# Kernel tuning notes

Measured on AMD Instinct MI355X. Metric: run time of the kernel, lower is better.

## Reference

```python
import jax, jax.numpy as jnp
import numpy as np

ENT_SIZE = 100000; REL_SIZE = 500; ENT_DIM = 256; REL_DIM = 256; H = 256
E = 2048; S = 32; N = 1024; THRESHOLD = 1.0; EPS = 1e-5


def _xav(k, shape):
    fan_in = shape[-1]
    fan_out = shape[-2] if len(shape) > 1 else shape[-1]
    std = (2.0 / (fan_in + fan_out)) ** 0.5
    return jax.random.normal(k, shape, jnp.float32) * std


def setup_inputs() -> dict:
    key = jax.random.key(0)
    ks = jax.random.split(key, 16)
    inp = {}
    inp["neighbors"] = jax.random.randint(ks[0], (E, S), 0, ENT_SIZE)
    inp["pos_h"] = jax.random.randint(ks[1], (N,), 0, E)
    inp["pos_t"] = jax.random.randint(ks[2], (N,), 0, E)
    inp["pos_r"] = jax.random.randint(ks[3], (N,), 0, REL_SIZE)
    inp["neg_h"] = jax.random.randint(ks[4], (N,), 0, E)
    inp["neg_t"] = jax.random.randint(ks[5], (N,), 0, E)
    inp["neg_r"] = jax.random.randint(ks[6], (N,), 0, REL_SIZE)
    inp["ent_embed"] = _xav(ks[7], (ENT_SIZE + 1, ENT_DIM))
    inp["rel_embed"] = _xav(ks[8], (REL_SIZE, REL_DIM))
    inp["trans"] = _xav(ks[9], (2 * REL_SIZE, REL_DIM, ENT_DIM))
    inp["W_ih_f"] = _xav(ks[10], (4 * H, ENT_DIM)); inp["W_hh_f"] = _xav(ks[11], (4 * H, H))
    inp["W_ih_b"] = _xav(ks[12], (4 * H, ENT_DIM)); inp["W_hh_b"] = _xav(ks[13], (4 * H, H))
    inp["b_f"] = jnp.zeros((4 * H,), jnp.float32)
    inp["b_b"] = jnp.zeros((4 * H,), jnp.float32)
    inp["W_lin"] = _xav(ks[14], (ENT_DIM, 2 * H)); inp["b_lin"] = jnp.zeros((ENT_DIM,), jnp.float32)
    inp["gamma"] = jnp.ones((ENT_DIM,), jnp.float32); inp["beta"] = jnp.zeros((ENT_DIM,), jnp.float32)
    return inp


def _lstm_final(x, W_ih, W_hh, b):
    # x: [E,S,D] -> final hidden state [E,H] (PyTorch LSTM gate order i,f,g,o; b = b_ih+b_hh)
    h0 = jnp.zeros((x.shape[0], H), x.dtype)
    def step(carry, xt):
        h, c = carry
        g = xt @ W_ih.T + h @ W_hh.T + b  # [E,4H]
        i, f, gg, o = jnp.split(g, 4, axis=-1)
        c = jax.nn.sigmoid(f) * c + jax.nn.sigmoid(i) * jnp.tanh(gg)
        h = jax.nn.sigmoid(o) * jnp.tanh(c)
        return (h, c), None
    (h, _), _ = jax.lax.scan(step, (h0, h0), jnp.swapaxes(x, 0, 1))
    return h


def _context(ent_embed, neighbors, W_ih_f, W_hh_f, b_f, W_ih_b, W_hh_b, b_b, W_lin, b_lin, gamma, beta):
    x_seq = ent_embed[neighbors]  # [E,S,D]
    h_f = _lstm_final(x_seq, W_ih_f, W_hh_f, b_f)
    h_b = _lstm_final(x_seq[:, ::-1], W_ih_b, W_hh_b, b_b)
    lin = jnp.concatenate([h_f, h_b], -1) @ W_lin.T + b_lin  # [E,ENT_DIM]
    # BatchNorm1d in training mode: batch stats (biased variance)
    mu = lin.mean(0)
    var = lin.var(0)
    return jnp.tanh(gamma * (lin - mu) * jax.lax.rsqrt(var + EPS) + beta)


def _score(trans, rel_embed, ctx, h_idx, r_idx, t_idx):
    Wh = trans[r_idx]             # [N,REL_DIM,ENT_DIM] (grouped expert GEMV, batched)
    Wt = trans[r_idx + REL_SIZE]
    d = jnp.einsum('nre,ne->nr', Wh, ctx[h_idx]) - jnp.einsum('nre,ne->nr', Wt, ctx[t_idx])
    return jnp.linalg.norm(d + rel_embed[r_idx], axis=1)


def reference(neighbors, pos_h, pos_t, pos_r, neg_h, neg_t, neg_r,
              ent_embed, rel_embed, trans, W_ih_f, W_hh_f, W_ih_b, W_hh_b,
              b_f, b_b, W_lin, b_lin, gamma, beta):
    ctx = _context(ent_embed, neighbors, W_ih_f, W_hh_f, b_f, W_ih_b, W_hh_b, b_b,
                   W_lin, b_lin, gamma, beta)
    pos_n = _score(trans, rel_embed, ctx, pos_h, pos_r, pos_t)
    neg_n = _score(trans, rel_embed, ctx, neg_h, neg_r, neg_t)
    return jnp.sum(pos_n + jax.nn.relu(THRESHOLD - neg_n))
```

## Files before the change

### kernel.cpp

```cpp
#include <hip/hip_runtime.h>

constexpr int kE   = 2048;
constexpr int kS   = 32;
constexpr int kD   = 256;
constexpr int kK   = 512;
constexpr int kREL = 500;
constexpr int kN   = 1024;

typedef unsigned short u16;
typedef __attribute__((ext_vector_type(8))) _Float16 f16x8;
typedef __attribute__((ext_vector_type(4))) float    f32x4;
typedef __attribute__((ext_vector_type(4))) unsigned short us4;

static __device__ __forceinline__ u16 f2h(float f) {
  _Float16 h = (_Float16)f;
  return __builtin_bit_cast(u16, h);
}
static __device__ __forceinline__ float h2f(u16 v) {
  _Float16 h = __builtin_bit_cast(_Float16, v);
  return (float)h;
}
static __device__ __forceinline__ float sigf(float x) { return 1.f / (1.f + __expf(-x)); }
static __device__ __forceinline__ float tanhfast(float x) {
  float e = __expf(2.f * x);
  return 1.f - 2.f / (e + 1.f);
}

__global__ void prep_weights(const float* __restrict__ Wih_f, const float* __restrict__ Whh_f,
                             const float* __restrict__ Wih_b, const float* __restrict__ Whh_b,
                             const float* __restrict__ Wlin_in,
                             u16* __restrict__ Wihr, u16* __restrict__ Whhr,
                             u16* __restrict__ Wlin) {
  int idx = blockIdx.x * 256 + threadIdx.x;
  if (idx < 65536) {
    int d = idx >> 15;
    int j = (idx & 32767) >> 5;
    int k = (idx & 31) * 8;
    int g = (j >> 4) & 3, u = (j >> 6) * 16 + (j & 15);
    int R = g * 256 + u;
    const float* src = (d ? Wih_b : Wih_f) + R * 256 + k;
    ushort oa[8];
#pragma unroll
    for (int i = 0; i < 8; i++) oa[i] = f2h(src[i]);
    *(uint4*)((char*)Wihr + (size_t)idx * 16) = *(uint4*)oa;
  } else if (idx < 131072) {
    int i2 = idx - 65536;
    int d = i2 >> 15;
    int j = (i2 & 32767) >> 5;
    int k = (i2 & 31) * 8;
    int g = (j >> 4) & 3, u = (j >> 6) * 16 + (j & 15);
    int R = g * 256 + u;
    const float* src = (d ? Whh_b : Whh_f) + R * 256 + k;
    ushort oa[8];
#pragma unroll
    for (int i = 0; i < 8; i++) oa[i] = f2h(src[i]);
    *(uint4*)((char*)Whhr + (size_t)i2 * 16) = *(uint4*)oa;
  } else if (idx < 131072 + 16384) {
    int q = (idx - 131072) * 8;
#pragma unroll
    for (int i = 0; i < 8; i++) Wlin[q + i] = f2h(Wlin_in[q + i]);
  }
}

__global__ void gather_x(const int* __restrict__ neighbors, const float* __restrict__ ent,
                         u16* __restrict__ x16) {
  const int tot = kS * kE * kD / 4;
  for (int i = blockIdx.x * blockDim.x + threadIdx.x; i < tot; i += gridDim.x * blockDim.x) {
    int k4 = i & 63;
    int row = i >> 6;
    int e = row & (kE - 1);
    int s = row >> 11;
    int nb = neighbors[e * kS + s];
    float4 v = *(const float4*)(ent + (size_t)nb * kD + k4 * 4);
    ushort4 o;
    o.x = f2h(v.x); o.y = f2h(v.y); o.z = f2h(v.z); o.w = f2h(v.w);
    *(ushort4*)(x16 + (size_t)row * kD + k4 * 4) = o;
  }
}

__global__ __launch_bounds__(256) void xgemm(
    const u16* __restrict__ x16, const u16* __restrict__ Wihr,
    const float* __restrict__ b_f, const float* __restrict__ b_b,
    u16* __restrict__ gx, int t0, int T) {
  const int tid = threadIdx.x, lane = tid & 63, w = tid >> 6;
  const int l15 = lane & 15, lq = lane >> 4;
  const int row0 = blockIdx.x * 64;
  const int y = blockIdx.y;
  const int dir = blockIdx.z;
  const int tt = row0 >> 11;
  const int e0 = row0 & 2047;
  const int s = dir ? (31 - (t0 + tt)) : (t0 + tt);
  const u16* Ab = x16 + ((size_t)s * kE + e0) * kD;
  const int c0 = y * 256 + w * 64;
  const u16* Bb = Wihr + ((size_t)dir * 1024 + c0) * kD;
  const float* bd = dir ? b_b : b_f;
  const int u = (c0 >> 6) * 16 + l15;

  f32x4 acc[4][4];
#pragma unroll
  for (int n = 0; n < 4; n++) {
    float bv = bd[n * 256 + u];
#pragma unroll
    for (int m = 0; m < 4; m++) acc[m][n] = (f32x4){bv, bv, bv, bv};
  }

  const int klane = lq * 8;
#pragma unroll
  for (int ks = 0; ks < 8; ks++) {
    const int ka = ks * 32 + klane;
    f16x8 a[4], b[4];
#pragma unroll
    for (int m = 0; m < 4; m++)
      a[m] = *(const f16x8*)(Ab + (size_t)(m * 16 + l15) * kD + ka);
#pragma unroll
    for (int n = 0; n < 4; n++)
      b[n] = *(const f16x8*)(Bb + (size_t)(n * 16 + l15) * kD + ka);
#pragma unroll
    for (int m = 0; m < 4; m++)
#pragma unroll
      for (int n = 0; n < 4; n++)
        acc[m][n] = __builtin_amdgcn_mfma_f32_16x16x32_f16(a[m], b[n], acc[m][n], 0, 0, 0);
  }

  u16* out = gx + (((size_t)dir * T + tt) * kE) * 1024;
#pragma unroll
  for (int m = 0; m < 4; m++)
#pragma unroll
    for (int r = 0; r < 4; r++) {
      int e = e0 + m * 16 + lq * 4 + r;
      us4 o;
      o[0] = f2h(acc[m][0][r]); o[1] = f2h(acc[m][1][r]);
      o[2] = f2h(acc[m][2][r]); o[3] = f2h(acc[m][3][r]);
      __builtin_nontemporal_store(o, (us4*)(out + ((size_t)e * 256 + u) * 4));
    }
}

__global__ __launch_bounds__(256) void lstm_step(
    const u16* __restrict__ gx, const u16* __restrict__ Whhr,
    const u16* __restrict__ hprev, u16* __restrict__ hnext,
    float* __restrict__ cbuf, int tt, int T) {
  const int tid = threadIdx.x, lane = tid & 63, w = tid >> 6;
  const int l15 = lane & 15, lq = lane >> 4;
  const int bid = blockIdx.x;
  const int dir = bid >> 8;
  const int rem = bid & 255;
  const int jg = rem >> 6;
  const int et = rem & 63;
  const int e0 = et * 32;
  const int c0 = jg * 256 + w * 64;
  const int unit = (c0 >> 6) * 16 + l15;

  const u16* Wd  = Whhr + ((size_t)dir * 1024 + c0) * kD;
  const u16* hpd = hprev + (size_t)dir * kE * kD;
  u16* hnd = hnext + (size_t)dir * kE * kD;
  float* cd = cbuf + (size_t)dir * kE * kD;
  const u16* gp = gx + ((size_t)dir * T + tt) * kE * 1024;

  f32x4 acc[2][4];
#pragma unroll
  for (int m = 0; m < 2; m++)
#pragma unroll
    for (int r = 0; r < 4; r++) {
      us4 g = __builtin_nontemporal_load(
          (const us4*)(gp + (size_t)(e0 + m * 16 + lq * 4 + r) * 1024 + unit * 4));
#pragma unroll
      for (int n = 0; n < 4; n++) acc[m][n][r] = h2f(g[n]);
    }

  const int klane = lq * 8;
#pragma unroll
  for (int ks = 0; ks < 8; ks++) {
    const int ka = ks * 32 + klane;
    f16x8 a[2], b[4];
#pragma unroll
    for (int m = 0; m < 2; m++)
      a[m] = *(const f16x8*)(hpd + (size_t)(e0 + m * 16 + l15) * kD + ka);
#pragma unroll
    for (int n = 0; n < 4; n++)
      b[n] = *(const f16x8*)(Wd + (size_t)(n * 16 + l15) * kD + ka);
#pragma unroll
    for (int m = 0; m < 2; m++)
#pragma unroll
      for (int n = 0; n < 4; n++)
        acc[m][n] = __builtin_amdgcn_mfma_f32_16x16x32_f16(a[m], b[n], acc[m][n], 0, 0, 0);
  }

#pragma unroll
  for (int m = 0; m < 2; m++)
#pragma unroll
    for (int r = 0; r < 4; r++) {
      int row = e0 + m * 16 + lq * 4 + r;
      size_t off = (size_t)row * kD + unit;
      float gi = acc[m][0][r];
      float gf = acc[m][1][r];
      float gg = acc[m][2][r];
      float go = acc[m][3][r];
      float c_old = cd[off];
      float cn = sigf(gf) * c_old + sigf(gi) * tanhfast(gg);
      cd[off] = cn;
      hnd[off] = f2h(sigf(go) * tanhfast(cn));
    }
}

static __device__ __forceinline__ void gemm_tile(
    const u16* __restrict__ Alo, const u16* __restrict__ Ahi,
    const u16* __restrict__ W, int e0,
    u16* As, u16* Bs, f32x4 (&acc)[4][4]) {
  const int tid = threadIdx.x;
  const int lane = tid & 63;
  const int w = tid >> 6;
#pragma unroll
  for (int m = 0; m < 4; m++)
#pragma unroll
    for (int n = 0; n < 4; n++) acc[m][n] = (f32x4){0.f, 0.f, 0.f, 0.f};

  for (int ch = 0; ch < 8; ++ch) {
    const int k0 = ch * 64;
    __syncthreads();
    const u16* Asrc = (k0 < 256) ? Alo : Ahi;
    const int kbase = (k0 < 256) ? k0 : (k0 - 256);
#pragma unroll
    for (int i = 0; i < 2; i++) {
      int idx = tid + i * 256;
      int row = idx >> 3, c8 = idx & 7;
      uint4 v = *(const uint4*)(Asrc + (size_t)(e0 + row) * 256 + kbase + c8 * 8);
      *(uint4*)((char*)As + row * 128 + ((c8 * 16) ^ ((row & 7) << 4))) = v;
    }
#pragma unroll
    for (int i = 0; i < 8; i++) {
      int idx = tid + i * 256;
      int j = idx >> 3, c8 = idx & 7;
      uint4 v = *(const uint4*)(W + (size_t)j * kK + k0 + c8 * 8);
      *(uint4*)((char*)Bs + j * 128 + ((c8 * 16) ^ ((j & 7) << 4))) = v;
    }
    __syncthreads();
#pragma unroll
    for (int ks = 0; ks < 2; ++ks) {
      const int kb = ks * 64 + (lane >> 4) * 16;
      f16x8 a[4], b[4];
#pragma unroll
      for (int m = 0; m < 4; m++) {
        int row = m * 16 + (lane & 15);
        a[m] = *(const f16x8*)((const char*)As + row * 128 + (kb ^ ((row & 7) << 4)));
      }
#pragma unroll
      for (int n = 0; n < 4; n++) {
        int row = w * 64 + n * 16 + (lane & 15);
        b[n] = *(const f16x8*)((const char*)Bs + row * 128 + (kb ^ ((row & 7) << 4)));
      }
#pragma unroll
      for (int m = 0; m < 4; m++)
#pragma unroll
        for (int n = 0; n < 4; n++)
          acc[m][n] = __builtin_amdgcn_mfma_f32_16x16x32_f16(a[m], b[n], acc[m][n], 0, 0, 0);
    }
  }
}

__global__ __launch_bounds__(256) void lin_kernel(
    const u16* __restrict__ hf, const u16* __restrict__ hb,
    const u16* __restrict__ Wl, const float* __restrict__ b_lin,
    float* __restrict__ lin) {
  __shared__ __align__(16) char smem[40960];
  u16* As = (u16*)smem;
  u16* Bs = (u16*)(smem + 8192);
  const int tid = threadIdx.x, lane = tid & 63, w = tid >> 6;
  const int e0 = blockIdx.x * 64;
  f32x4 acc[4][4];
  gemm_tile(hf, hb, Wl, e0, As, Bs, acc);
#pragma unroll
  for (int m = 0; m < 4; m++)
#pragma unroll
    for (int n = 0; n < 4; n++)
#pragma unroll
      for (int r = 0; r < 4; r++) {
        int e = e0 + m * 16 + (lane >> 4) * 4 + r;
        int col = w * 64 + n * 16 + (lane & 15);
        lin[(size_t)e * 256 + col] = acc[m][n][r] + b_lin[col];
      }
}

__global__ void bn_stats(const float* __restrict__ lin, float* __restrict__ part) {
  int b = blockIdx.x, c = threadIdx.x;
  float s = 0.f, s2 = 0.f;
  for (int e = b * 32; e < b * 32 + 32; ++e) {
    float x = lin[(size_t)e * 256 + c];
    s += x; s2 += x * x;
  }
  part[b * 256 + c] = s;
  part[64 * 256 + b * 256 + c] = s2;
}

__global__ void bn_apply(const float* __restrict__ lin, const float* __restrict__ part,
                         const float* __restrict__ gamma, const float* __restrict__ beta,
                         float* __restrict__ ctx) {
  int c = threadIdx.x;
  float s = 0.f, s2 = 0.f;
  for (int b = 0; b < 64; b++) { s += part[b * 256 + c]; s2 += part[64 * 256 + b * 256 + c]; }
  float mu = s * (1.f / 2048.f);
  float rsig = rsqrtf(s2 * (1.f / 2048.f) - mu * mu + 1e-5f);
  float ga = gamma[c], be = beta[c];
  int e0 = blockIdx.x * 8;
  for (int e = e0; e < e0 + 8; ++e) {
    float x = lin[(size_t)e * 256 + c];
    ctx[(size_t)e * 256 + c] = tanhf(ga * (x - mu) * rsig + be);
  }
}

__global__ void group_rel(const int* __restrict__ pr, const int* __restrict__ nr,
                          int* __restrict__ offs, int* __restrict__ list) {
  __shared__ int cnt[512], sc[512], cur[512];
  int tid = threadIdx.x;
  cnt[tid] = 0;
  __syncthreads();
  for (int i = tid; i < 2 * kN; i += 512) {
    int r = (i < kN) ? pr[i] : nr[i - kN];
    atomicAdd(&cnt[r], 1);
  }
  __syncthreads();
  sc[tid] = cnt[tid];
  __syncthreads();
  for (int d = 1; d < 512; d <<= 1) {
    int v = (tid >= d) ? sc[tid - d] : 0;
    __syncthreads();
    sc[tid] += v;
    __syncthreads();
  }
  int excl = (tid == 0) ? 0 : sc[tid - 1];
  cur[tid] = excl;
  if (tid <= kREL) offs[tid] = excl;
  __syncthreads();
  for (int i = tid; i < 2 * kN; i += 512) {
    int r = (i < kN) ? pr[i] : nr[i - kN];
    int p = atomicAdd(&cur[r], 1);
    list[p] = i;
  }
}

__global__ __launch_bounds__(256) void score_grouped(
    const float* __restrict__ ctx, const float* __restrict__ trans,
    const float* __restrict__ rel_embed,
    const int* __restrict__ ph, const int* __restrict__ pt,
    const int* __restrict__ nh, const int* __restrict__ nt,
    const int* __restrict__ offs, const int* __restrict__ list,
    float* __restrict__ scores) {
  int r = blockIdx.x;
  int start = offs[r], end = offs[r + 1];
  if (start >= end) return;
  int tid = threadIdx.x;
  __shared__ float cs[8][2][256];
  __shared__ float red[8][4];
  float relv = rel_embed[r * 256 + tid];
  const float4* Whp = (const float4*)(trans + (size_t)r * 65536 + (size_t)tid * 256);
  const float4* Wtp = (const float4*)(trans + ((size_t)r + kREL) * 65536 + (size_t)tid * 256);

  for (int chunk = start; chunk < end; chunk += 8) {
    int G = min(8, end - chunk);
    for (int j = 0; j < G; j++) {
      int i = list[chunk + j];
      int hh = (i < kN) ? ph[i] : nh[i - kN];
      int tt = (i < kN) ? pt[i] : nt[i - kN];
      cs[j][0][tid] = ctx[(size_t)hh * 256 + tid];
      cs[j][1][tid] = ctx[(size_t)tt * 256 + tid];
    }
    __syncthreads();
    float acc[8];
#pragma unroll
    for (int j = 0; j < 8; j++) acc[j] = relv;
#pragma unroll 2
    for (int q = 0; q < 64; q++) {
      float4 w1 = Whp[q];
      float4 w2 = Wtp[q];
#pragma unroll
      for (int j = 0; j < 8; j++) {
        float4 xh = *(const float4*)&cs[j][0][q * 4];
        float4 xt = *(const float4*)&cs[j][1][q * 4];
        acc[j] += w1.x * xh.x + w1.y * xh.y + w1.z * xh.z + w1.w * xh.w
                - (w2.x * xt.x + w2.y * xt.y + w2.z * xt.z + w2.w * xt.w);
      }
    }
    for (int j = 0; j < G; j++) {
      float sq = acc[j] * acc[j];
      for (int o = 32; o; o >>= 1) sq += __shfl_down(sq, o);
      if ((tid & 63) == 0) red[j][tid >> 6] = sq;
    }
    __syncthreads();
    if (tid < G) {
      float s = red[tid][0] + red[tid][1] + red[tid][2] + red[tid][3];
      scores[list[chunk + tid]] = sqrtf(s);
    }
    __syncthreads();
  }
}

__global__ void final_reduce(const float* __restrict__ scores, float* __restrict__ out) {
  int tid = threadIdx.x;
  float a = 0.f;
  for (int i = tid; i < 2 * kN; i += 256) {
    float s = scores[i];
    a += (i < kN) ? s : fmaxf(0.f, 1.f - s);
  }
  for (int off = 32; off; off >>= 1) a += __shfl_down(a, off);
  __shared__ float w4[4];
  if ((tid & 63) == 0) w4[tid >> 6] = a;
  __syncthreads();
  if (tid == 0) out[0] = w4[0] + w4[1] + w4[2] + w4[3];
}

extern "C" void kernel_launch(void* const* d_in, const int* in_sizes, int n_in,
                              void* d_out, int out_size, void* d_ws, size_t ws_size,
                              hipStream_t stream) {
  const int*   neighbors = (const int*)d_in[0];
  const int*   pos_h = (const int*)d_in[1];
  const int*   pos_t = (const int*)d_in[2];
  const int*   pos_r = (const int*)d_in[3];
  const int*   neg_h = (const int*)d_in[4];
  const int*   neg_t = (const int*)d_in[5];
  const int*   neg_r = (const int*)d_in[6];
  const float* ent_embed = (const float*)d_in[7];
  const float* rel_embed = (const float*)d_in[8];
  const float* trans = (const float*)d_in[9];
  const float* W_ih_f = (const float*)d_in[10];
  const float* W_hh_f = (const float*)d_in[11];
  const float* W_ih_b = (const float*)d_in[12];
  const float* W_hh_b = (const float*)d_in[13];
  const float* b_f = (const float*)d_in[14];
  const float* b_b = (const float*)d_in[15];
  const float* W_lin = (const float*)d_in[16];
  const float* b_lin = (const float*)d_in[17];
  const float* gamma = (const float*)d_in[18];
  const float* beta = (const float*)d_in[19];

  char* ws = (char*)d_ws;
  size_t off = 0;
  auto alloc = [&](size_t bytes) {
    void* p = ws + off;
    off = (off + bytes + 255) & ~(size_t)255;
    return p;
  };
  u16* Wihr   = (u16*)alloc((size_t)2 * 1024 * kD * 2);
  u16* Whhr   = (u16*)alloc((size_t)2 * 1024 * kD * 2);
  u16* Wlin   = (u16*)alloc((size_t)256 * kK * 2);
  u16* x16    = (u16*)alloc((size_t)kS * kE * kD * 2);
  u16* h0     = (u16*)alloc((size_t)2 * kE * kD * 2);
  u16* h1     = (u16*)alloc((size_t)2 * kE * kD * 2);
  float* cbuf = (float*)alloc((size_t)2 * kE * kD * 4);
  float* lin  = (float*)alloc((size_t)kE * 256 * 4);
  float* part = (float*)alloc((size_t)2 * 64 * 256 * 4);
  float* ctx  = (float*)alloc((size_t)kE * 256 * 4);
  float* scores = (float*)alloc((size_t)2 * kN * 4);
  int* offsb  = (int*)alloc((size_t)512 * 4);
  int* list   = (int*)alloc((size_t)2 * kN * 4);
  size_t fixed_end = off;
  (void)in_sizes; (void)n_in; (void)out_size;

  int T = 2;
  for (int cand = 32; cand >= 2; cand >>= 1) {
    size_t gxb = (size_t)2 * cand * kE * 1024 * 2;
    if (fixed_end + gxb + (1 << 20) <= ws_size) { T = cand; break; }
  }
  u16* gx = (u16*)alloc((size_t)2 * T * kE * 1024 * 2);

  hipMemsetAsync(h0, 0, (size_t)2 * kE * kD * 2, stream);
  hipMemsetAsync(cbuf, 0, (size_t)2 * kE * kD * 4, stream);

  prep_weights<<<576, 256, 0, stream>>>(W_ih_f, W_hh_f, W_ih_b, W_hh_b, W_lin,
                                        Wihr, Whhr, Wlin);
  gather_x<<<4096, 256, 0, stream>>>(neighbors, ent_embed, x16);
  group_rel<<<1, 512, 0, stream>>>(pos_r, neg_r, offsb, list);

  for (int t0 = 0; t0 < kS; t0 += T) {
    xgemm<<<dim3(T * 32, 4, 2), 256, 0, stream>>>(x16, Wihr, b_f, b_b, gx, t0, T);
    for (int tt = 0; tt < T; tt++) {
      int t = t0 + tt;
      const u16* hp = (t & 1) ? h1 : h0;
      u16* hn = (t & 1) ? h0 : h1;
      lstm_step<<<512, 256, 0, stream>>>(gx, Whhr, hp, hn, cbuf, tt, T);
    }
  }

  lin_kernel<<<32, 256, 0, stream>>>(h0, h0 + (size_t)kE * kD, Wlin, b_lin, lin);
  bn_stats<<<64, 256, 0, stream>>>(lin, part);
  bn_apply<<<256, 256, 0, stream>>>(lin, part, gamma, beta, ctx);
  score_grouped<<<kREL, 256, 0, stream>>>(ctx, trans, rel_embed,
                                          pos_h, pos_t, neg_h, neg_t, offsb, list, scores);
  final_reduce<<<1, 256, 0, stream>>>(scores, (float*)d_out);
}
```

Before: 951.6 us.

## Stage xgemm operands through LDS via pre-swizzled tile images

The input gather and the W_ih prep now write pre-tiled, XOR-swizzled images, so each 64-row by 64-k chunk is contiguous. xgemm loads these chunks straight into shared memory with global_load_lds and reads MFMA fragments from LDS using the swizzle, instead of doing strided per-lane global loads. The aim is coalesced loads, B-tile reuse across the four waves through LDS, and fewer bank conflicts. In exchange it adds syncthreads per k-chunk with no double buffering, and more complex index layouts in the prep kernels.

```diff
diff --git a/kernel.cpp b/kernel.cpp
--- a/kernel.cpp
+++ b/kernel.cpp
@@ -25,24 +25,33 @@
   float e = __expf(2.f * x);
   return 1.f - 2.f / (e + 1.f);
 }
+static __device__ __forceinline__ void gl_lds16(const void* g, void* l) {
+  __builtin_amdgcn_global_load_lds((const __attribute__((address_space(1))) unsigned int*)g,
+                                   (__attribute__((address_space(3))) unsigned int*)l, 16, 0, 0);
+}
 
 __global__ void prep_weights(const float* __restrict__ Wih_f, const float* __restrict__ Whh_f,
                              const float* __restrict__ Wih_b, const float* __restrict__ Whh_b,
                              const float* __restrict__ Wlin_in,
-                             u16* __restrict__ Wihr, u16* __restrict__ Whhr,
+                             u16* __restrict__ Wv3, u16* __restrict__ Whhr,
                              u16* __restrict__ Wlin) {
   int idx = blockIdx.x * 256 + threadIdx.x;
   if (idx < 65536) {
-    int d = idx >> 15;
-    int j = (idx & 32767) >> 5;
-    int k = (idx & 31) * 8;
-    int g = (j >> 4) & 3, u = (j >> 6) * 16 + (j & 15);
+    int q  = idx & 2047;
+    int ch = (idx >> 11) & 3;
+    int y  = (idx >> 13) & 3;
+    int d  = idx >> 15;
+    int j  = q >> 3;
+    int k8 = (q & 7) ^ (j & 7);
+    int jg = y * 256 + j;
+    int g = (jg >> 4) & 3, u = (jg >> 6) * 16 + (jg & 15);
     int R = g * 256 + u;
+    int k = ch * 64 + k8 * 8;
     const float* src = (d ? Wih_b : Wih_f) + R * 256 + k;
     ushort oa[8];
 #pragma unroll
     for (int i = 0; i < 8; i++) oa[i] = f2h(src[i]);
-    *(uint4*)((char*)Wihr + (size_t)idx * 16) = *(uint4*)oa;
+    *(uint4*)((char*)Wv3 + (size_t)idx * 16) = *(uint4*)oa;
   } else if (idx < 131072) {
     int i2 = idx - 65536;
     int d = i2 >> 15;
@@ -63,38 +72,44 @@
 }
 
 __global__ void gather_x(const int* __restrict__ neighbors, const float* __restrict__ ent,
-                         u16* __restrict__ x16) {
-  const int tot = kS * kE * kD / 4;
-  for (int i = blockIdx.x * blockDim.x + threadIdx.x; i < tot; i += gridDim.x * blockDim.x) {
-    int k4 = i & 63;
-    int row = i >> 6;
-    int e = row & (kE - 1);
-    int s = row >> 11;
-    int nb = neighbors[e * kS + s];
-    float4 v = *(const float4*)(ent + (size_t)nb * kD + k4 * 4);
-    ushort4 o;
-    o.x = f2h(v.x); o.y = f2h(v.y); o.z = f2h(v.z); o.w = f2h(v.w);
-    *(ushort4*)(x16 + (size_t)row * kD + k4 * 4) = o;
-  }
+                         u16* __restrict__ ximg) {
+  int idx = blockIdx.x * 256 + threadIdx.x;
+  int q    = idx & 511;
+  int ch   = (idx >> 9) & 3;
+  int tile = (idx >> 11) & 31;
+  int s    = idx >> 16;
+  int row = q >> 3;
+  int c8 = (q & 7) ^ (row & 7);
+  int e = tile * 64 + row;
+  int k = ch * 64 + c8 * 8;
+  int nb = neighbors[e * 32 + s];
+  const float* src = ent + (size_t)nb * 256 + k;
+  float4 v0 = *(const float4*)src;
+  float4 v1 = *(const float4*)(src + 4);
+  ushort oa[8];
+  oa[0] = f2h(v0.x); oa[1] = f2h(v0.y); oa[2] = f2h(v0.z); oa[3] = f2h(v0.w);
+  oa[4] = f2h(v1.x); oa[5] = f2h(v1.y); oa[6] = f2h(v1.z); oa[7] = f2h(v1.w);
+  *(uint4*)((char*)ximg + (size_t)idx * 16) = *(uint4*)oa;
 }
 
 __global__ __launch_bounds__(256) void xgemm(
-    const u16* __restrict__ x16, const u16* __restrict__ Wihr,
+    const u16* __restrict__ ximg, const u16* __restrict__ Wv3,
     const float* __restrict__ b_f, const float* __restrict__ b_b,
     u16* __restrict__ gx, int t0, int T) {
+  __shared__ __align__(16) char As[8192];
+  __shared__ __align__(16) char Bs[32768];
   const int tid = threadIdx.x, lane = tid & 63, w = tid >> 6;
   const int l15 = lane & 15, lq = lane >> 4;
   const int row0 = blockIdx.x * 64;
-  const int y = blockIdx.y;
-  const int dir = blockIdx.z;
+  const int y = blockIdx.y, dir = blockIdx.z;
   const int tt = row0 >> 11;
   const int e0 = row0 & 2047;
+  const int etile = e0 >> 6;
   const int s = dir ? (31 - (t0 + tt)) : (t0 + tt);
-  const u16* Ab = x16 + ((size_t)s * kE + e0) * kD;
-  const int c0 = y * 256 + w * 64;
-  const u16* Bb = Wihr + ((size_t)dir * 1024 + c0) * kD;
+  const char* imgA = (const char*)ximg + (size_t)(s * 32 + etile) * 32768;
+  const char* imgB = (const char*)Wv3 + (size_t)(dir * 4 + y) * 131072;
   const float* bd = dir ? b_b : b_f;
-  const int u = (c0 >> 6) * 16 + l15;
+  const int u = (y * 4 + w) * 16 + l15;
 
   f32x4 acc[4][4];
 #pragma unroll
@@ -104,22 +119,37 @@
     for (int m = 0; m < 4; m++) acc[m][n] = (f32x4){bv, bv, bv, bv};
   }
 
-  const int klane = lq * 8;
-#pragma unroll
-  for (int ks = 0; ks < 8; ks++) {
-    const int ka = ks * 32 + klane;
-    f16x8 a[4], b[4];
-#pragma unroll
-    for (int m = 0; m < 4; m++)
-      a[m] = *(const f16x8*)(Ab + (size_t)(m * 16 + l15) * kD + ka);
-#pragma unroll
-    for (int n = 0; n < 4; n++)
-      b[n] = *(const f16x8*)(Bb + (size_t)(n * 16 + l15) * kD + ka);
-#pragma unroll
-    for (int m = 0; m < 4; m++)
-#pragma unroll
-      for (int n = 0; n < 4; n++)
-        acc[m][n] = __builtin_amdgcn_mfma_f32_16x16x32_f16(a[m], b[n], acc[m][n], 0, 0, 0);
+  for (int ch = 0; ch < 4; ++ch) {
+#pragma unroll
+    for (int i = 0; i < 2; i++)
+      gl_lds16(imgA + ch * 8192 + i * 4096 + w * 1024 + lane * 16,
+               As + i * 4096 + w * 1024);
+#pragma unroll
+    for (int i = 0; i < 8; i++)
+      gl_lds16(imgB + (size_t)ch * 32768 + i * 4096 + w * 1024 + lane * 16,
+               Bs + i * 4096 + w * 1024);
+    __syncthreads();
+#pragma unroll
+    for (int ks = 0; ks < 2; ++ks) {
+      const int kb = ks * 64 + lq * 16;
+      f16x8 a[4], b[4];
+#pragma unroll
+      for (int m = 0; m < 4; m++) {
+        int row = m * 16 + l15;
+        a[m] = *(const f16x8*)(As + row * 128 + (kb ^ ((row & 7) << 4)));
+      }
+#pragma unroll
+      for (int n = 0; n < 4; n++) {
+        int row = w * 64 + n * 16 + l15;
+        b[n] = *(const f16x8*)(Bs + row * 128 + (kb ^ ((row & 7) << 4)));
+      }
+#pragma unroll
+      for (int m = 0; m < 4; m++)
+#pragma unroll
+        for (int n = 0; n < 4; n++)
+          acc[m][n] = __builtin_amdgcn_mfma_f32_16x16x32_f16(a[m], b[n], acc[m][n], 0, 0, 0);
+    }
+    __syncthreads();
   }
 
   u16* out = gx + (((size_t)dir * T + tt) * kE) * 1024;
@@ -438,10 +468,10 @@
     off = (off + bytes + 255) & ~(size_t)255;
     return p;
   };
-  u16* Wihr   = (u16*)alloc((size_t)2 * 1024 * kD * 2);
+  u16* Wv3    = (u16*)alloc((size_t)65536 * 16);
   u16* Whhr   = (u16*)alloc((size_t)2 * 1024 * kD * 2);
   u16* Wlin   = (u16*)alloc((size_t)256 * kK * 2);
-  u16* x16    = (u16*)alloc((size_t)kS * kE * kD * 2);
+  u16* ximg   = (u16*)alloc((size_t)2097152 * 16);
   u16* h0     = (u16*)alloc((size_t)2 * kE * kD * 2);
   u16* h1     = (u16*)alloc((size_t)2 * kE * kD * 2);
   float* cbuf = (float*)alloc((size_t)2 * kE * kD * 4);
@@ -465,12 +495,12 @@
   hipMemsetAsync(cbuf, 0, (size_t)2 * kE * kD * 4, stream);
 
   prep_weights<<<576, 256, 0, stream>>>(W_ih_f, W_hh_f, W_ih_b, W_hh_b, W_lin,
-                                        Wihr, Whhr, Wlin);
-  gather_x<<<4096, 256, 0, stream>>>(neighbors, ent_embed, x16);
+                                        Wv3, Whhr, Wlin);
+  gather_x<<<8192, 256, 0, stream>>>(neighbors, ent_embed, ximg);
   group_rel<<<1, 512, 0, stream>>>(pos_r, neg_r, offsb, list);
 
   for (int t0 = 0; t0 < kS; t0 += T) {
-    xgemm<<<dim3(T * 32, 4, 2), 256, 0, stream>>>(x16, Wihr, b_f, b_b, gx, t0, T);
+    xgemm<<<dim3(T * 32, 4, 2), 256, 0, stream>>>(ximg, Wv3, b_f, b_b, gx, t0, T);
     for (int tt = 0; tt < T; tt++) {
       int t = t0 + tt;
       const u16* hp = (t & 1) ? h1 : h0;
```

Result: faster. 831.4 us (-12.6%).
